# Kernel optimization log

Hardware: AMD Instinct MI355X
Metric: run time of the kernel (lower is better)

Reference implementation:

```python
import jax, jax.numpy as jnp
import numpy as np

LN_EPS = 1e-5


def _layernorm(x, gamma, beta):
    mu = jnp.mean(x, axis=-1, keepdims=True)
    var = jnp.mean(jnp.square(x - mu), axis=-1, keepdims=True)
    return (x - mu) * jax.lax.rsqrt(var + LN_EPS) * gamma + beta


def setup_inputs() -> dict:
    key = jax.random.key(0)
    ks = jax.random.split(key, 8)
    B, T, C, H, HS = 8, 2048, 384, 6, 64
    s = C ** -0.5
    return {
        "x": jax.random.normal(ks[0], (B, T, C), jnp.float32),
        "wq": jax.random.normal(ks[1], (H, C, HS), jnp.float32) * s,
        "wk": jax.random.normal(ks[2], (H, C, HS), jnp.float32) * s,
        "wv": jax.random.normal(ks[3], (H, C, HS), jnp.float32) * s,
        "w_proj": jax.random.normal(ks[4], (C, C), jnp.float32) * s,
        "b_proj": jnp.zeros((C,), jnp.float32),
        "w1": jax.random.normal(ks[5], (C, 4 * C), jnp.float32) * s,
        "b1": jnp.zeros((4 * C,), jnp.float32),
        "w2": jax.random.normal(ks[6], (4 * C, C), jnp.float32) * (4 * C) ** -0.5,
        "b2": jnp.zeros((C,), jnp.float32),
        "g1": jnp.ones((C,), jnp.float32),
        "be1": jnp.zeros((C,), jnp.float32),
        "g2": jnp.ones((C,), jnp.float32),
        "be2": jnp.zeros((C,), jnp.float32),
    }


def reference(x, wq, wk, wv, w_proj, b_proj, w1, b1, w2, b2, g1, be1, g2, be2):
    B, T, C = x.shape
    HS = wq.shape[-1]
    # --- multi-head causal self-attention (per-head linear, concat, proj) ---
    q = jnp.einsum("btc,hcd->bhtd", x, wq)
    k = jnp.einsum("btc,hcd->bhtd", x, wk)
    v = jnp.einsum("btc,hcd->bhtd", x, wv)
    scores = jnp.einsum("bhtd,bhsd->bhts", q, k) * (HS ** -0.5)
    causal = jnp.tril(jnp.ones((T, T), bool))
    scores = jnp.where(causal, scores, -jnp.inf)
    att = jax.nn.softmax(scores, axis=-1)  # dropout = identity (eval)
    o = jnp.einsum("bhts,bhsd->bhtd", att, v)
    o = o.transpose(0, 2, 1, 3).reshape(B, T, C)  # concat heads
    sa = o @ w_proj + b_proj
    # --- post-LN residual ---
    x = _layernorm(x + sa, g1, be1)
    # --- feed-forward ---
    ff = jax.nn.relu(x @ w1 + b1) @ w2 + b2
    x = _layernorm(x + ff, g2, be2)
    return x
```

## Files before the change

kernel.cpp:

```cpp
#include <hip/hip_runtime.h>

typedef unsigned short u16;
typedef unsigned int u32;
typedef u16 u16x4 __attribute__((ext_vector_type(4)));
typedef u16 u16x8 __attribute__((ext_vector_type(8)));
typedef u32 u32x4 __attribute__((ext_vector_type(4)));
typedef __bf16 bf16v8 __attribute__((ext_vector_type(8)));
typedef float f32x4 __attribute__((ext_vector_type(4)));
typedef float f32x2 __attribute__((ext_vector_type(2)));

#define DEV __device__ __forceinline__

DEV u16 f2bf(float f) {
  union { float f; u32 u; } v; v.f = f;
  u32 r = v.u + 0x7fffu + ((v.u >> 16) & 1u);
  return (u16)(r >> 16);
}
DEV float bf2f(u16 u) { union { u32 u; float f; } v; v.u = ((u32)u) << 16; return v.f; }

DEV u32 cvtpk(float a, float b) {
  u32 d;
  asm("v_cvt_pk_bf16_f32 %0, %1, %2" : "=v"(d) : "v"(a), "v"(b));
  return d;
}

DEV f32x4 mfma16(u16x8 a, u16x8 b, f32x4 c) {
  return __builtin_amdgcn_mfma_f32_16x16x32_bf16(
      __builtin_bit_cast(bf16v8, a), __builtin_bit_cast(bf16v8, b), c, 0, 0, 0);
}

typedef const __attribute__((address_space(1))) void* gas_ptr;
typedef __attribute__((address_space(3))) void* las_ptr;
#define GLOAD16(GP, LP) __builtin_amdgcn_global_load_lds((gas_ptr)(GP), (las_ptr)(LP), 16, 0, 0)

__global__ __launch_bounds__(256) void cast_x_kernel(const float* __restrict__ x,
                                                     u16* __restrict__ xb) {
  int i = blockIdx.x * 256 + threadIdx.x;
  const f32x4* p = (const f32x4*)x;
  f32x4 a = p[2 * i], b = p[2 * i + 1];
  u16x8 o;
  #pragma unroll
  for (int j = 0; j < 4; ++j) { o[j] = f2bf(a[j]); o[4 + j] = f2bf(b[j]); }
  *((u16x8*)xb + i) = o;
}

__global__ __launch_bounds__(256) void prep_w_kernel(
    const float* __restrict__ wq, const float* __restrict__ wk,
    const float* __restrict__ wv, const float* __restrict__ wproj,
    const float* __restrict__ w1, const float* __restrict__ w2,
    u16* __restrict__ wqkvt, u16* __restrict__ wprojt,
    u16* __restrict__ w1t, u16* __restrict__ w2t) {
  int idx = blockIdx.x * 256 + threadIdx.x;
  if (idx < 442368) {
    int n = idx / 384, c = idx % 384;
    int which = n / 384;
    int hd = n % 384;
    int h = hd >> 6, d = hd & 63;
    const float* src = (which == 0) ? wq : ((which == 1) ? wk : wv);
    wqkvt[idx] = f2bf(src[((size_t)h * 384 + c) * 64 + d]);
  } else if (idx < 442368 + 147456) {
    int e = idx - 442368;
    int n = e / 384, c = e % 384;
    wprojt[e] = f2bf(wproj[(size_t)c * 384 + n]);
  } else if (idx < 442368 + 147456 + 589824) {
    int e = idx - (442368 + 147456);
    int n = e / 384, c = e % 384;
    w1t[e] = f2bf(w1[(size_t)c * 1536 + n]);
  } else {
    int e = idx - (442368 + 147456 + 589824);
    int n = e / 1536, c = e % 1536;
    w2t[e] = f2bf(w2[(size_t)c * 384 + n]);
  }
}

template <int K, int EPI>
__global__ __launch_bounds__(256) void gemm_kernel(
    const u16* __restrict__ A, const u16* __restrict__ Bt, const int N,
    const float* __restrict__ bias, const float* __restrict__ resf,
    const u16* __restrict__ resb, void* __restrict__ outv, void* __restrict__ outv2) {
  __shared__ u16 As[2 * 64 * 64];
  __shared__ u16 Bs[2 * 128 * 64];
  const int t = threadIdx.x;
  const int w = t >> 6, l = t & 63, l15 = l & 15, lg = l >> 4;
  const int wcol = w * 32;
  const int m0 = blockIdx.x * 64, n0 = blockIdx.y * 128;
  const int lr8 = l >> 3;
  const int su = (l & 7) ^ lr8;
  const u16* gA = A + (size_t)(m0 + lr8) * K + su * 8;
  const u16* gB = Bt + (size_t)(n0 + lr8) * K + su * 8;

  f32x4 acc[4][2];
  #pragma unroll
  for (int i = 0; i < 4; ++i)
    #pragma unroll
    for (int j = 0; j < 2; ++j) acc[i][j] = (f32x4){0.f, 0.f, 0.f, 0.f};

  auto stage = [&](int kt, int buf) {
    #pragma unroll
    for (int c = 0; c < 2; ++c)
      GLOAD16(gA + (size_t)(w * 16 + c * 8) * K + kt * 64,
              (char*)As + buf * 8192 + w * 2048 + c * 1024);
    #pragma unroll
    for (int c = 0; c < 4; ++c)
      GLOAD16(gB + (size_t)(w * 32 + c * 8) * K + kt * 64,
              (char*)Bs + buf * 16384 + w * 4096 + c * 1024);
  };

  constexpr int NT = K / 64;
  int cur = 0;
  stage(0, 0);
  #pragma unroll 1
  for (int kt = 0; kt < NT; ++kt) {
    __syncthreads();
    if (kt + 1 < NT) stage(kt + 1, cur ^ 1);
    const u16* Ab = As + cur * 4096;
    const u16* Bb = Bs + cur * 8192;
    u16x8 af[4][2], bfr[2][2];
    #pragma unroll
    for (int i = 0; i < 4; ++i) {
      const int row = i * 16 + l15;
      #pragma unroll
      for (int ks = 0; ks < 2; ++ks)
        af[i][ks] = *(const u16x8*)&Ab[row * 64 + (((4 * ks + lg) ^ (row & 7)) << 3)];
    }
    #pragma unroll
    for (int j = 0; j < 2; ++j) {
      const int row = wcol + j * 16 + l15;
      #pragma unroll
      for (int ks = 0; ks < 2; ++ks)
        bfr[j][ks] = *(const u16x8*)&Bb[row * 64 + (((4 * ks + lg) ^ (row & 7)) << 3)];
    }
    #pragma unroll
    for (int ks = 0; ks < 2; ++ks)
      #pragma unroll
      for (int mi = 0; mi < 4; ++mi)
        #pragma unroll
        for (int ni = 0; ni < 2; ++ni)
          acc[mi][ni] = mfma16(af[mi][ks], bfr[ni][ks], acc[mi][ni]);
    cur ^= 1;
  }

  #pragma unroll
  for (int mi = 0; mi < 4; ++mi) {
    #pragma unroll
    for (int ni = 0; ni < 2; ++ni) {
      const int rowg = m0 + mi * 16 + lg * 4;
      const int colg = n0 + wcol + ni * 16 + l15;
      if constexpr (EPI == 0) {
        if (n0 < 768) {
          #pragma unroll
          for (int r = 0; r < 4; ++r)
            ((u16*)outv)[(size_t)(rowg + r) * 768 + colg] = f2bf(acc[mi][ni][r]);
        } else {
          const int hd = colg - 768;
          u16x4 pv;
          #pragma unroll
          for (int r = 0; r < 4; ++r) pv[r] = f2bf(acc[mi][ni][r]);
          *(u16x4*)((u16*)outv2 + (size_t)((rowg >> 11) * 6 + (hd >> 6)) * 131072 +
                    (size_t)(hd & 63) * 2048 + (rowg & 2047)) = pv;
        }
      } else {
        const float b_ = bias[colg];
        #pragma unroll
        for (int r = 0; r < 4; ++r) {
          float v = acc[mi][ni][r];
          const size_t oi = (size_t)(rowg + r) * N + colg;
          if constexpr (EPI == 1) {
            ((float*)outv)[oi] = v + b_ + resf[oi];
          } else if constexpr (EPI == 2) {
            ((u16*)outv)[oi] = f2bf(fmaxf(v + b_, 0.f));
          } else {
            ((float*)outv)[oi] = v + b_ + bf2f(resb[oi]);
          }
        }
      }
    }
  }
}

__global__ __launch_bounds__(256, 5) void attn_kernel(const u16* __restrict__ qk,
                                                      const u16* __restrict__ vt,
                                                      u16* __restrict__ o,
                                                      float* __restrict__ part) {
  __shared__ __align__(16) char smem[32768];

  const int t = threadIdx.x;
  const int w = t >> 6, l = t & 63, l15 = l & 15, lg = l >> 4;
  const int idx = blockIdx.x;
  const int hl = idx % 48;
  const int g = idx / 48;
  int qt, k0, k1, e = 0;
  bool heavy;
  if (g < 32) {
    heavy = true; e = g;
    qt = 31 - (g >> 1);
    const int kmid = (qt + 1) >> 1;
    if (g & 1) { k0 = kmid; k1 = qt + 1; } else { k0 = 0; k1 = kmid; }
  } else {
    heavy = false; qt = 47 - g; k0 = 0; k1 = qt + 1;
  }
  const int b = hl / 6, head = hl % 6;
  const float SC = 0.125f * 1.44269504f;
  const float FM = 17.312340f;

  u16x8 qf[2];
  {
    const u16* qp = qk + (size_t)b * 2048 * 768 +
                    (size_t)(qt * 64 + w * 16 + l15) * 768 + head * 64 + lg * 8;
    qf[0] = *(const u16x8*)qp;
    qf[1] = *(const u16x8*)(qp + 32);
  }
  u16x8 ones;
  #pragma unroll
  for (int j = 0; j < 8; ++j) ones[j] = 0x3F80;

  f32x4 Oa[4];
  f32x4 Osum = (f32x4){0.f, 0.f, 0.f, 0.f};
  #pragma unroll
  for (int i = 0; i < 4; ++i) Oa[i] = (f32x4){0.f, 0.f, 0.f, 0.f};

  const int su16 = ((l & 7) ^ (l >> 3)) << 4;
  const char* kg0 = (const char*)qk + (size_t)b * 2048 * 1536 +
                    (size_t)(w * 8 + (l >> 3)) * 1536 + (size_t)(384 + head * 64) * 2 + su16;
  const char* vg0 = (const char*)vt + (size_t)(b * 6 + head) * 262144 +
                    (size_t)(w * 8 + (l >> 3)) * 4096 + su16;

  auto stage = [&](int kt, int bufsel) {
    const char* kg = kg0 + (size_t)kt * 98304;
    const char* vg = vg0 + (size_t)kt * 128;
    char* kl = smem + bufsel * 8192 + w * 1024;
    char* vl = smem + 16384 + bufsel * 8192 + w * 1024;
    GLOAD16(kg, kl);
    GLOAD16(kg + 49152, kl + 4096);
    GLOAD16(vg, vl);
    GLOAD16(vg + 131072, vl + 4096);
  };

  auto compute = [&](int bufoff, bool diag) {
    f32x4 sa[4];
    __builtin_amdgcn_s_setprio(1);
    #pragma unroll
    for (int st = 0; st < 4; ++st) {
      sa[st] = (f32x4){0.f, 0.f, 0.f, 0.f};
      const int sr = st * 16 + l15;
      #pragma unroll
      for (int ks = 0; ks < 2; ++ks) {
        u16x8 kf = *(const u16x8*)(smem + bufoff + sr * 128 +
                                   (((ks * 4 + lg) ^ (sr & 7)) << 4));
        sa[st] = mfma16(kf, qf[ks], sa[st]);
      }
    }
    __builtin_amdgcn_s_setprio(0);
    if (diag) {
      #pragma unroll
      for (int st = 0; st < 4; ++st)
        #pragma unroll
        for (int r = 0; r < 4; ++r)
          if (st * 16 + lg * 4 + r > w * 16 + l15) sa[st][r] = -3.0e38f;
    }
    u32 pk2[4][2];
    #pragma unroll
    for (int st = 0; st < 4; ++st) {
      float e0 = exp2f(sa[st][0] * SC - FM);
      float e1 = exp2f(sa[st][1] * SC - FM);
      float e2 = exp2f(sa[st][2] * SC - FM);
      float e3 = exp2f(sa[st][3] * SC - FM);
      pk2[st][0] = cvtpk(e0, e1);
      pk2[st][1] = cvtpk(e2, e3);
    }
    #pragma unroll
    for (int ks = 0; ks < 2; ++ks) {
      u32 wds[4];
      #pragma unroll
      for (int wd = 0; wd < 4; ++wd) {
        int src = ((2 * (lg & 1) + (wd >> 1)) << 4) | l15;
        u32 c0 = (u32)__shfl((int)pk2[2 * ks][wd & 1], src);
        u32 c1 = (u32)__shfl((int)pk2[2 * ks + 1][wd & 1], src);
        wds[wd] = (lg & 2) ? c1 : c0;
      }
      u16x8 pf = __builtin_bit_cast(u16x8, (u32x4){wds[0], wds[1], wds[2], wds[3]});
      __builtin_amdgcn_s_setprio(1);
      #pragma unroll
      for (int dt = 0; dt < 4; ++dt) {
        const int dd = dt * 16 + l15;
        u16x8 vf = *(const u16x8*)(smem + 16384 + bufoff + dd * 128 +
                                   (((ks * 4 + lg) ^ (dd & 7)) << 4));
        Oa[dt] = mfma16(pf, vf, Oa[dt]);
      }
      Osum = mfma16(pf, ones, Osum);
      __builtin_amdgcn_s_setprio(0);
    }
  };

  int cur = 0;
  stage(k0, 0);
  #pragma unroll 1
  for (int kt = k0; kt < k1; ++kt) {
    __syncthreads();
    if (kt + 1 < k1) stage(kt + 1, cur ^ 1);
    compute(cur * 8192, kt == qt);
    cur ^= 1;
  }

  if (!heavy) {
    float inv[4];
    #pragma unroll
    for (int r = 0; r < 4; ++r) inv[r] = 1.0f / Osum[r];
    #pragma unroll
    for (int dt = 0; dt < 4; ++dt)
      #pragma unroll
      for (int r = 0; r < 4; ++r) {
        size_t row = (size_t)b * 2048 + qt * 64 + w * 16 + lg * 4 + r;
        o[row * 384 + head * 64 + dt * 16 + l15] = f2bf(Oa[dt][r] * inv[r]);
      }
  } else {
    float* slot = part + (size_t)(hl * 32 + e) * 4224;
    if (l15 == 0) {
      #pragma unroll
      for (int r = 0; r < 4; ++r) slot[w * 16 + lg * 4 + r] = Osum[r];
    }
    #pragma unroll
    for (int dt = 0; dt < 4; ++dt)
      #pragma unroll
      for (int r = 0; r < 4; ++r)
        slot[128 + (w * 16 + lg * 4 + r) * 64 + dt * 16 + l15] = Oa[dt][r];
  }
}

__global__ __launch_bounds__(256) void attn_combine_kernel(const float* __restrict__ part,
                                                           u16* __restrict__ o) {
  const int idx = blockIdx.x;
  const int hl = idx % 48;
  const int qt = 31 - idx / 48;
  const int e0 = (31 - qt) * 2;
  const float* s0 = part + (size_t)(hl * 32 + e0) * 4224;
  const float* s1 = s0 + 4224;
  const int t = threadIdx.x;
  const int row = t >> 2, c0 = (t & 3) * 16;
  const float inv = 1.0f / (s0[row] + s1[row]);
  const int b = hl / 6, head = hl % 6;
  const f32x4* a0 = (const f32x4*)(s0 + 128 + row * 64 + c0);
  const f32x4* a1 = (const f32x4*)(s1 + 128 + row * 64 + c0);
  u32 wv[8];
  #pragma unroll
  for (int j = 0; j < 4; ++j) {
    f32x4 va = a0[j], vb = a1[j];
    float y0 = (va[0] + vb[0]) * inv;
    float y1 = (va[1] + vb[1]) * inv;
    float y2 = (va[2] + vb[2]) * inv;
    float y3 = (va[3] + vb[3]) * inv;
    wv[2 * j] = cvtpk(y0, y1);
    wv[2 * j + 1] = cvtpk(y2, y3);
  }
  u16* op = o + ((size_t)(b * 2048 + qt * 64 + row)) * 384 + head * 64 + c0;
  *(u32x4*)op = (u32x4){wv[0], wv[1], wv[2], wv[3]};
  *(u32x4*)(op + 8) = (u32x4){wv[4], wv[5], wv[6], wv[7]};
}

template <int OUT_BF16>
__global__ __launch_bounds__(256) void ln_kernel(const float* __restrict__ in,
                                                 const float* __restrict__ g,
                                                 const float* __restrict__ be,
                                                 void* __restrict__ outv) {
  const int row = blockIdx.x * 4 + (threadIdx.x >> 6);
  const int lane = threadIdx.x & 63;
  const float* p = in + (size_t)row * 384 + lane * 6;
  float v[6];
  {
    const f32x2* p2 = (const f32x2*)p;
    f32x2 a0 = p2[0], a1 = p2[1], a2 = p2[2];
    v[0] = a0[0]; v[1] = a0[1]; v[2] = a1[0]; v[3] = a1[1]; v[4] = a2[0]; v[5] = a2[1];
  }
  float s = v[0] + v[1] + v[2] + v[3] + v[4] + v[5];
  #pragma unroll
  for (int m = 1; m < 64; m <<= 1) s += __shfl_xor(s, m, 64);
  const float mu = s * (1.0f / 384.0f);
  float d2 = 0.f;
  #pragma unroll
  for (int j = 0; j < 6; ++j) { float d = v[j] - mu; d2 += d * d; }
  #pragma unroll
  for (int m = 1; m < 64; m <<= 1) d2 += __shfl_xor(d2, m, 64);
  const float rstd = rsqrtf(d2 * (1.0f / 384.0f) + 1e-5f);
  const int c = lane * 6;
  float y[6];
  #pragma unroll
  for (int j = 0; j < 6; ++j) y[j] = (v[j] - mu) * rstd * g[c + j] + be[c + j];
  if constexpr (OUT_BF16) {
    u32* ob = (u32*)((u16*)outv + (size_t)row * 384 + c);
    #pragma unroll
    for (int j = 0; j < 3; ++j)
      ob[j] = (u32)f2bf(y[2 * j]) | ((u32)f2bf(y[2 * j + 1]) << 16);
  } else {
    float* of = (float*)outv + (size_t)row * 384 + c;
    f32x2* o2 = (f32x2*)of;
    #pragma unroll
    for (int j = 0; j < 3; ++j) o2[j] = (f32x2){y[2 * j], y[2 * j + 1]};
  }
}

extern "C" void kernel_launch(void* const* d_in, const int* in_sizes, int n_in,
                              void* d_out, int out_size, void* d_ws, size_t ws_size,
                              hipStream_t stream) {
  const float* x     = (const float*)d_in[0];
  const float* wq    = (const float*)d_in[1];
  const float* wk    = (const float*)d_in[2];
  const float* wv    = (const float*)d_in[3];
  const float* wproj = (const float*)d_in[4];
  const float* bproj = (const float*)d_in[5];
  const float* w1    = (const float*)d_in[6];
  const float* b1    = (const float*)d_in[7];
  const float* w2    = (const float*)d_in[8];
  const float* b2    = (const float*)d_in[9];
  const float* g1    = (const float*)d_in[10];
  const float* be1   = (const float*)d_in[11];
  const float* g2    = (const float*)d_in[12];
  const float* be2   = (const float*)d_in[13];

  char* ws = (char*)d_ws;
  u16*   xb    = (u16*)(ws + 0);
  u16*   qk    = (u16*)(ws + 12582912);
  u16*   vt    = (u16*)(ws + 37748736);
  u16*   obuf  = (u16*)(ws + 50331648);
  float* res1  = (float*)(ws + 62914560);
  u16*   x1b   = (u16*)(ws + 88080384);
  u16*   wqkvt = (u16*)(ws + 100663296);
  u16*   wprjt = (u16*)(ws + 101548032);
  u16*   w1t   = (u16*)(ws + 101842944);
  u16*   w2t   = (u16*)(ws + 103022592);
  u16*   h1    = qk;
  float* part  = res1;

  cast_x_kernel<<<3072, 256, 0, stream>>>(x, xb);
  prep_w_kernel<<<6912, 256, 0, stream>>>(wq, wk, wv, wproj, w1, w2, wqkvt, wprjt, w1t, w2t);
  gemm_kernel<384, 0><<<dim3(256, 9), 256, 0, stream>>>(xb, wqkvt, 768, nullptr, nullptr, nullptr, qk, vt);
  attn_kernel<<<2304, 256, 0, stream>>>(qk, vt, obuf, part);
  attn_combine_kernel<<<768, 256, 0, stream>>>(part, obuf);
  gemm_kernel<384, 1><<<dim3(256, 3), 256, 0, stream>>>(obuf, wprjt, 384, bproj, x, nullptr, res1, nullptr);
  ln_kernel<1><<<4096, 256, 0, stream>>>(res1, g1, be1, x1b);
  gemm_kernel<384, 2><<<dim3(256, 12), 256, 0, stream>>>(x1b, w1t, 1536, b1, nullptr, nullptr, h1, nullptr);
  gemm_kernel<1536, 3><<<dim3(256, 3), 256, 0, stream>>>(h1, w2t, 384, b2, nullptr, x1b, res1, nullptr);
  ln_kernel<0><<<4096, 256, 0, stream>>>(res1, g2, be2, d_out);
}
```

Measured before the change: 207.7 us.

## Stage GEMM epilogues through LDS, store residuals in bf16, merge prep kernels

GEMM epilogues now write bias-added (and ReLU'd) results as bf16 into an LDS tile and then emit coalesced 16-byte stores. Residual adds now read bf16 residuals (xb, x1b) rather than fp32 x, and the pre-LayerNorm sums are written as bf16 instead of fp32. LayerNorm reads bf16 input, and the x cast and weight prep are merged into one launch. This cuts global memory traffic and launch count, at the cost of extra bf16 rounding on residual paths: the input x is now rounded before the first residual add, and the sums are rounded before normalization.

Result: faster. 191.4 us (-7.9%).

```diff
diff --git a/kernel.cpp b/kernel.cpp
--- a/kernel.cpp
+++ b/kernel.cpp
@@ -17,6 +17,8 @@
   return (u16)(r >> 16);
 }
 DEV float bf2f(u16 u) { union { u32 u; float f; } v; v.u = ((u32)u) << 16; return v.f; }
+DEV float bfu32lo(u32 w) { union { u32 u; float f; } v; v.u = w << 16; return v.f; }
+DEV float bfu32hi(u32 w) { union { u32 u; float f; } v; v.u = w & 0xffff0000u; return v.f; }
 
 DEV u32 cvtpk(float a, float b) {
   u32 d;
@@ -33,24 +35,25 @@
 typedef __attribute__((address_space(3))) void* las_ptr;
 #define GLOAD16(GP, LP) __builtin_amdgcn_global_load_lds((gas_ptr)(GP), (las_ptr)(LP), 16, 0, 0)
 
-__global__ __launch_bounds__(256) void cast_x_kernel(const float* __restrict__ x,
-                                                     u16* __restrict__ xb) {
-  int i = blockIdx.x * 256 + threadIdx.x;
-  const f32x4* p = (const f32x4*)x;
-  f32x4 a = p[2 * i], b = p[2 * i + 1];
-  u16x8 o;
-  #pragma unroll
-  for (int j = 0; j < 4; ++j) { o[j] = f2bf(a[j]); o[4 + j] = f2bf(b[j]); }
-  *((u16x8*)xb + i) = o;
-}
-
-__global__ __launch_bounds__(256) void prep_w_kernel(
+__global__ __launch_bounds__(256) void prep_kernel(
+    const float* __restrict__ x, u16* __restrict__ xb,
     const float* __restrict__ wq, const float* __restrict__ wk,
     const float* __restrict__ wv, const float* __restrict__ wproj,
     const float* __restrict__ w1, const float* __restrict__ w2,
     u16* __restrict__ wqkvt, u16* __restrict__ wprojt,
     u16* __restrict__ w1t, u16* __restrict__ w2t) {
-  int idx = blockIdx.x * 256 + threadIdx.x;
+  const int bid = blockIdx.x;
+  if (bid < 3072) {
+    int i = bid * 256 + threadIdx.x;
+    const f32x4* p = (const f32x4*)x;
+    f32x4 a = p[2 * i], b = p[2 * i + 1];
+    u16x8 o;
+    #pragma unroll
+    for (int j = 0; j < 4; ++j) { o[j] = f2bf(a[j]); o[4 + j] = f2bf(b[j]); }
+    *((u16x8*)xb + i) = o;
+    return;
+  }
+  int idx = (bid - 3072) * 256 + threadIdx.x;
   if (idx < 442368) {
     int n = idx / 384, c = idx % 384;
     int which = n / 384;
@@ -76,10 +79,11 @@
 template <int K, int EPI>
 __global__ __launch_bounds__(256) void gemm_kernel(
     const u16* __restrict__ A, const u16* __restrict__ Bt, const int N,
-    const float* __restrict__ bias, const float* __restrict__ resf,
-    const u16* __restrict__ resb, void* __restrict__ outv, void* __restrict__ outv2) {
-  __shared__ u16 As[2 * 64 * 64];
-  __shared__ u16 Bs[2 * 128 * 64];
+    const float* __restrict__ bias, const u16* __restrict__ resb,
+    void* __restrict__ outv, void* __restrict__ outv2) {
+  __shared__ u16 sm[24576];
+  u16* As = sm;
+  u16* Bs = sm + 8192;
   const int t = threadIdx.x;
   const int w = t >> 6, l = t & 63, l15 = l & 15, lg = l >> 4;
   const int wcol = w * 32;
@@ -140,40 +144,54 @@
     cur ^= 1;
   }
 
-  #pragma unroll
-  for (int mi = 0; mi < 4; ++mi) {
+  __syncthreads();
+  if (EPI == 0 && n0 >= 768) {
+    #pragma unroll
+    for (int mi = 0; mi < 4; ++mi)
+      #pragma unroll
+      for (int ni = 0; ni < 2; ++ni) {
+        const int rowg = m0 + mi * 16 + lg * 4;
+        const int hd = n0 + wcol + ni * 16 + l15 - 768;
+        u16x4 pv;
+        #pragma unroll
+        for (int r = 0; r < 4; ++r) pv[r] = f2bf(acc[mi][ni][r]);
+        *(u16x4*)((u16*)outv2 + (size_t)((rowg >> 11) * 6 + (hd >> 6)) * 131072 +
+                  (size_t)(hd & 63) * 2048 + (rowg & 2047)) = pv;
+      }
+    return;
+  }
+  u16* Wl = sm + w * 4096;
+  #pragma unroll
+  for (int mi = 0; mi < 4; ++mi)
     #pragma unroll
     for (int ni = 0; ni < 2; ++ni) {
-      const int rowg = m0 + mi * 16 + lg * 4;
-      const int colg = n0 + wcol + ni * 16 + l15;
-      if constexpr (EPI == 0) {
-        if (n0 < 768) {
-          #pragma unroll
-          for (int r = 0; r < 4; ++r)
-            ((u16*)outv)[(size_t)(rowg + r) * 768 + colg] = f2bf(acc[mi][ni][r]);
-        } else {
-          const int hd = colg - 768;
-          u16x4 pv;
-          #pragma unroll
-          for (int r = 0; r < 4; ++r) pv[r] = f2bf(acc[mi][ni][r]);
-          *(u16x4*)((u16*)outv2 + (size_t)((rowg >> 11) * 6 + (hd >> 6)) * 131072 +
-                    (size_t)(hd & 63) * 2048 + (rowg & 2047)) = pv;
-        }
-      } else {
-        const float b_ = bias[colg];
-        #pragma unroll
-        for (int r = 0; r < 4; ++r) {
-          float v = acc[mi][ni][r];
-          const size_t oi = (size_t)(rowg + r) * N + colg;
-          if constexpr (EPI == 1) {
-            ((float*)outv)[oi] = v + b_ + resf[oi];
-          } else if constexpr (EPI == 2) {
-            ((u16*)outv)[oi] = f2bf(fmaxf(v + b_, 0.f));
-          } else {
-            ((float*)outv)[oi] = v + b_ + bf2f(resb[oi]);
-          }
-        }
-      }
+      float b_ = 0.f;
+      if constexpr (EPI != 0) b_ = bias[n0 + wcol + ni * 16 + l15];
+      #pragma unroll
+      for (int r = 0; r < 4; ++r) {
+        float v = acc[mi][ni][r] + b_;
+        if constexpr (EPI == 2) v = fmaxf(v, 0.f);
+        Wl[(mi * 16 + lg * 4 + r) * 40 + ni * 16 + l15] = f2bf(v);
+      }
+    }
+  asm volatile("s_waitcnt lgkmcnt(0)" ::: "memory");
+  __builtin_amdgcn_sched_barrier(0);
+  const int rcol = (l & 3) * 8;
+  #pragma unroll
+  for (int p = 0; p < 4; ++p) {
+    const int row = (l >> 2) + 16 * p;
+    u16x8 cv = *(const u16x8*)&Wl[row * 40 + rcol];
+    const size_t off = (size_t)(m0 + row) * N + n0 + wcol + rcol;
+    if constexpr (EPI == 1) {
+      u16x8 rv = *(const u16x8*)&resb[off];
+      u32 ov[4];
+      #pragma unroll
+      for (int j = 0; j < 4; ++j)
+        ov[j] = cvtpk(bf2f(cv[2 * j]) + bf2f(rv[2 * j]),
+                      bf2f(cv[2 * j + 1]) + bf2f(rv[2 * j + 1]));
+      *(u32x4*)((u16*)outv + off) = (u32x4){ov[0], ov[1], ov[2], ov[3]};
+    } else {
+      *(u16x8*)((u16*)outv + off) = cv;
     }
   }
 }
@@ -357,16 +375,22 @@
   *(u32x4*)(op + 8) = (u32x4){wv[4], wv[5], wv[6], wv[7]};
 }
 
-template <int OUT_BF16>
-__global__ __launch_bounds__(256) void ln_kernel(const float* __restrict__ in,
+template <int IN_BF16, int OUT_BF16>
+__global__ __launch_bounds__(256) void ln_kernel(const void* __restrict__ inv,
                                                  const float* __restrict__ g,
                                                  const float* __restrict__ be,
                                                  void* __restrict__ outv) {
   const int row = blockIdx.x * 4 + (threadIdx.x >> 6);
   const int lane = threadIdx.x & 63;
-  const float* p = in + (size_t)row * 384 + lane * 6;
   float v[6];
-  {
+  if constexpr (IN_BF16) {
+    const u16* pb = (const u16*)inv + (size_t)row * 384 + lane * 6;
+    u32 w0 = *(const u32*)pb, w1 = *(const u32*)(pb + 2), w2 = *(const u32*)(pb + 4);
+    v[0] = bfu32lo(w0); v[1] = bfu32hi(w0);
+    v[2] = bfu32lo(w1); v[3] = bfu32hi(w1);
+    v[4] = bfu32lo(w2); v[5] = bfu32hi(w2);
+  } else {
+    const float* p = (const float*)inv + (size_t)row * 384 + lane * 6;
     const f32x2* p2 = (const f32x2*)p;
     f32x2 a0 = p2[0], a1 = p2[1], a2 = p2[2];
     v[0] = a0[0]; v[1] = a0[1]; v[2] = a1[0]; v[3] = a1[1]; v[4] = a2[0]; v[5] = a2[1];
@@ -388,8 +412,7 @@
   if constexpr (OUT_BF16) {
     u32* ob = (u32*)((u16*)outv + (size_t)row * 384 + c);
     #pragma unroll
-    for (int j = 0; j < 3; ++j)
-      ob[j] = (u32)f2bf(y[2 * j]) | ((u32)f2bf(y[2 * j + 1]) << 16);
+    for (int j = 0; j < 3; ++j) ob[j] = cvtpk(y[2 * j], y[2 * j + 1]);
   } else {
     float* of = (float*)outv + (size_t)row * 384 + c;
     f32x2* o2 = (f32x2*)of;
@@ -421,23 +444,24 @@
   u16*   qk    = (u16*)(ws + 12582912);
   u16*   vt    = (u16*)(ws + 37748736);
   u16*   obuf  = (u16*)(ws + 50331648);
-  float* res1  = (float*)(ws + 62914560);
+  float* part  = (float*)(ws + 62914560);
   u16*   x1b   = (u16*)(ws + 88080384);
   u16*   wqkvt = (u16*)(ws + 100663296);
   u16*   wprjt = (u16*)(ws + 101548032);
   u16*   w1t   = (u16*)(ws + 101842944);
   u16*   w2t   = (u16*)(ws + 103022592);
+  u16*   r1b   = (u16*)(ws + 62914560);
   u16*   h1    = qk;
-  float* part  = res1;
-
-  cast_x_kernel<<<3072, 256, 0, stream>>>(x, xb);
-  prep_w_kernel<<<6912, 256, 0, stream>>>(wq, wk, wv, wproj, w1, w2, wqkvt, wprjt, w1t, w2t);
-  gemm_kernel<384, 0><<<dim3(256, 9), 256, 0, stream>>>(xb, wqkvt, 768, nullptr, nullptr, nullptr, qk, vt);
+  u16*   r2b   = xb;
+
+  prep_kernel<<<9984, 256, 0, stream>>>(x, xb, wq, wk, wv, wproj, w1, w2,
+                                        wqkvt, wprjt, w1t, w2t);
+  gemm_kernel<384, 0><<<dim3(256, 9), 256, 0, stream>>>(xb, wqkvt, 768, nullptr, nullptr, qk, vt);
   attn_kernel<<<2304, 256, 0, stream>>>(qk, vt, obuf, part);
   attn_combine_kernel<<<768, 256, 0, stream>>>(part, obuf);
-  gemm_kernel<384, 1><<<dim3(256, 3), 256, 0, stream>>>(obuf, wprjt, 384, bproj, x, nullptr, res1, nullptr);
-  ln_kernel<1><<<4096, 256, 0, stream>>>(res1, g1, be1, x1b);
-  gemm_kernel<384, 2><<<dim3(256, 12), 256, 0, stream>>>(x1b, w1t, 1536, b1, nullptr, nullptr, h1, nullptr);
-  gemm_kernel<1536, 3><<<dim3(256, 3), 256, 0, stream>>>(h1, w2t, 384, b2, nullptr, x1b, res1, nullptr);
-  ln_kernel<0><<<4096, 256, 0, stream>>>(res1, g2, be2, d_out);
-}
+  gemm_kernel<384, 1><<<dim3(256, 3), 256, 0, stream>>>(obuf, wprjt, 384, bproj, xb, r1b, nullptr);
+  ln_kernel<1, 1><<<4096, 256, 0, stream>>>(r1b, g1, be1, x1b);
+  gemm_kernel<384, 2><<<dim3(256, 12), 256, 0, stream>>>(x1b, w1t, 1536, b1, nullptr, h1, nullptr);
+  gemm_kernel<1536, 1><<<dim3(256, 3), 256, 0, stream>>>(h1, w2t, 384, b2, x1b, r2b, nullptr);
+  ln_kernel<1, 0><<<4096, 256, 0, stream>>>(r2b, g2, be2, d_out);
+}
```
